# Optimization experiments

Hardware: AMD Instinct MI355X
Metric: run time of the kernel (lower is better)

The kernel has to match this reference:

```python
import jax, jax.numpy as jnp
import numpy as np

H = 1024      # hidden_size
M = 64        # matrix_dim = int(sqrt(4096))
R = 2         # rank
LS = 2048     # local_size = budget_size // 2


def setup_inputs() -> dict:
    key = jax.random.key(0)
    ks = jax.random.split(key, 12)
    B, S = 4, 2048
    def lin(k, fan_in, fan_out):
        # stored as [in, out] so forward is x @ W
        return jax.random.normal(k, (fan_in, fan_out), dtype=jnp.float32) / np.sqrt(fan_in)
    return {
        "x": jax.random.normal(ks[0], (B, S, H), dtype=jnp.float32),
        "W_decay": lin(ks[1], H, 1),
        "W_key": lin(ks[2], H, R * M),
        "W_value": lin(ks[3], H, R * M),
        "W_ql": lin(ks[4], H, M),
        "W_qr": lin(ks[5], H, M),
        "W_rec_out": lin(ks[6], M, H),
        "W_up": lin(ks[7], H, LS),
        "W_gate": lin(ks[8], H, LS),
        "W_down": lin(ks[9], LS, H),
        "init_state": jnp.zeros((M, M), dtype=jnp.float32),
    }


def reference(x, W_decay, W_key, W_value, W_ql, W_qr, W_rec_out, W_up, W_gate, W_down, init_state):
    B, S, _ = x.shape
    # Precompute all per-token projections (vectorized over batch & seq)
    decay = jax.nn.sigmoid(x @ W_decay)[..., 0]            # [B,S]
    keys = (x @ W_key).reshape(B, S, R, M)                 # [B,S,R,M]
    values = (x @ W_value).reshape(B, S, R, M)             # [B,S,R,M]
    write = jnp.einsum('bsrm,bsrn->bsmn', keys, values) / float(R)  # [B,S,M,M]
    ql = x @ W_ql                                          # [B,S,M]
    qr = x @ W_qr                                          # [B,S,M]

    def step(state, inp):
        d, w, ql_t, qr_t = inp                             # d:[B], w:[B,M,M], ql/qr:[B,M]
        d3 = d[:, None, None]
        state = d3 * state + (1.0 - d3) * w                # decayed matrix-state update
        read = jnp.einsum('bm,bmn->bn', ql_t, state) * qr_t  # [B,M]
        return state, read

    state0 = jnp.broadcast_to(init_state, (B, M, M))
    # scan over time axis (time-major inputs)
    _, reads = jax.lax.scan(
        step, state0,
        (decay.transpose(1, 0), write.transpose(1, 0, 2, 3),
         ql.transpose(1, 0, 2), qr.transpose(1, 0, 2)))
    reads = reads.transpose(1, 0, 2)                       # [B,S,M]

    recurrent = jax.nn.silu(reads) @ W_rec_out             # [B,S,H]
    local = ((x @ W_up) * jax.nn.silu(x @ W_gate)) @ W_down  # SwiGLU branch
    return recurrent + local
```

## Files before the change

kernel.cpp:

```cpp
#include <hip/hip_runtime.h>
#include <hip/hip_bf16.h>

typedef __bf16 bf16x8 __attribute__((ext_vector_type(8)));
typedef float f32x4 __attribute__((ext_vector_type(4)));

#define BS   8192
#define Hd   1024
#define LSd  2048
#define Md   64

static __device__ __forceinline__ float bfu2f(unsigned short u) {
  return __uint_as_float(((unsigned int)u) << 16);
}
static __device__ __forceinline__ __hip_bfloat16 f2bf(float f) { return __float2bfloat16(f); }



__global__ __launch_bounds__(256) void conv_frag_kernel(const float* __restrict__ src,
    __hip_bfloat16* __restrict__ dst) {
  int wid = (blockIdx.x * 256 + threadIdx.x) >> 6;
  int lane = threadIdx.x & 63;
  int t = wid >> 3, ri = wid & 7;
  int mb = t >> 5, kt = t & 31;
  int row = mb * 128 + ri * 16 + (lane & 15);
  int k = kt * 32 + (lane >> 4) * 8;
  const float* s = src + (size_t)row * 1024 + k;
  float4 f0 = *(const float4*)s;
  float4 f1 = *(const float4*)(s + 4);
  union { unsigned short u8[8]; uint4 v; } o;
  o.u8[0] = __bfloat16_as_ushort(f2bf(f0.x)); o.u8[1] = __bfloat16_as_ushort(f2bf(f0.y));
  o.u8[2] = __bfloat16_as_ushort(f2bf(f0.z)); o.u8[3] = __bfloat16_as_ushort(f2bf(f0.w));
  o.u8[4] = __bfloat16_as_ushort(f2bf(f1.x)); o.u8[5] = __bfloat16_as_ushort(f2bf(f1.y));
  o.u8[6] = __bfloat16_as_ushort(f2bf(f1.z)); o.u8[7] = __bfloat16_as_ushort(f2bf(f1.w));
  *(uint4*)(dst + (size_t)wid * 512 + lane * 8) = o.v;
}

__global__ __launch_bounds__(256) void prep_wcat_frag_kernel(const float* __restrict__ Wd,
    const float* __restrict__ Wk, const float* __restrict__ Wv,
    const float* __restrict__ Wql, const float* __restrict__ Wqr,
    __hip_bfloat16* __restrict__ out) {
  int i = blockIdx.x * 256 + threadIdx.x;
  int t = i >> 12, ri = (i >> 9) & 7, l = (i >> 3) & 63, e = i & 7;
  int n = (t >> 5) * 128 + ri * 16 + (l & 15);
  int h = (t & 31) * 32 + (l >> 4) * 8 + e;
  float v = 0.f;
  if (n == 0)        v = Wd[h];
  else if (n < 129)  v = Wk[h * 128 + (n - 1)];
  else if (n < 257)  v = Wv[h * 128 + (n - 129)];
  else if (n < 321)  v = Wql[h * 64 + (n - 257)];
  else if (n < 385)  v = Wqr[h * 64 + (n - 321)];
  out[i] = f2bf(v);
}

__global__ __launch_bounds__(256) void transpose_frag_kernel(const float* __restrict__ src,
    __hip_bfloat16* __restrict__ dst, int Ktot, int Nsrc, int n_off) {
  __shared__ float tile[32][129];
  int kt = blockIdx.x, nb = blockIdx.y;
  int k0 = kt * 32, n0 = nb * 128;
  int tid = threadIdx.x;
  int kr = tid >> 3, nc = (tid & 7) * 16;
  const float* s = src + (size_t)(k0 + kr) * Nsrc + n0 + nc;
  #pragma unroll
  for (int u = 0; u < 16; u += 4) {
    float4 f = *(const float4*)(s + u);
    tile[kr][nc + u + 0] = f.x; tile[kr][nc + u + 1] = f.y;
    tile[kr][nc + u + 2] = f.z; tile[kr][nc + u + 3] = f.w;
  }
  __syncthreads();
  int wave = tid >> 6, lane = tid & 63;
  int tIdx = ((n0 + n_off) >> 7) * (Ktot >> 5) + kt;
  __hip_bfloat16* d = dst + ((size_t)tIdx << 12);
  #pragma unroll
  for (int it = 0; it < 2; ++it) {
    int ri = wave * 2 + it;
    int nl = ri * 16 + (lane & 15), kq = (lane >> 4) * 8;
    union { unsigned short u8[8]; uint4 v; } o;
    #pragma unroll
    for (int e = 0; e < 8; ++e)
      o.u8[e] = __bfloat16_as_ushort(f2bf(tile[kq + e][nl]));
    *(uint4*)(d + ri * 512 + lane * 8) = o.v;
  }
}


static __device__ __forceinline__ void stage_async_frag(const __hip_bfloat16* __restrict__ tile_src,
    __hip_bfloat16* __restrict__ dst, int wave, int lane) {
  #pragma unroll
  for (int it = 0; it < 2; ++it) {
    int ri = wave * 2 + it;
    __builtin_amdgcn_global_load_lds(
        (const __attribute__((address_space(1))) void*)(tile_src + ri * 512 + lane * 8),
        (__attribute__((address_space(3))) void*)(dst + ri * 512),
        16, 0, 0);
  }
}

static __device__ __forceinline__ void mfma_single(const __hip_bfloat16* sA, const __hip_bfloat16* sB,
    int wm16, int wn16, int lane, f32x4 acc[4][4]) {
  bf16x8 af[4], bg[4];
  #pragma unroll
  for (int i = 0; i < 4; ++i) af[i] = *(const bf16x8*)(sA + (wm16 + i) * 512 + lane * 8);
  #pragma unroll
  for (int j = 0; j < 4; ++j) bg[j] = *(const bf16x8*)(sB + (wn16 + j) * 512 + lane * 8);
  #pragma unroll
  for (int i = 0; i < 4; ++i)
    #pragma unroll
    for (int j = 0; j < 4; ++j)
      acc[i][j] = __builtin_amdgcn_mfma_f32_16x16x32_bf16(af[i], bg[j], acc[i][j], 0, 0, 0);
}

static __device__ __forceinline__ void mfma_dual(const __hip_bfloat16* sA,
    const __hip_bfloat16* sBu, const __hip_bfloat16* sBg,
    int wm16, int wn16, int lane, f32x4 accu[4][4], f32x4 accg[4][4]) {
  bf16x8 af[4], bu[4], bg[4];
  #pragma unroll
  for (int i = 0; i < 4; ++i) af[i] = *(const bf16x8*)(sA + (wm16 + i) * 512 + lane * 8);
  #pragma unroll
  for (int j = 0; j < 4; ++j) bu[j] = *(const bf16x8*)(sBu + (wn16 + j) * 512 + lane * 8);
  #pragma unroll
  for (int j = 0; j < 4; ++j) bg[j] = *(const bf16x8*)(sBg + (wn16 + j) * 512 + lane * 8);
  #pragma unroll
  for (int i = 0; i < 4; ++i)
    #pragma unroll
    for (int j = 0; j < 4; ++j) {
      accu[i][j] = __builtin_amdgcn_mfma_f32_16x16x32_bf16(af[i], bu[j], accu[i][j], 0, 0, 0);
      accg[i][j] = __builtin_amdgcn_mfma_f32_16x16x32_bf16(af[i], bg[j], accg[i][j], 0, 0, 0);
    }
}

__global__ __launch_bounds__(256, 2) void gemm_proj_kernel(const __hip_bfloat16* __restrict__ A,
    const __hip_bfloat16* __restrict__ Bt, float* __restrict__ C) {
  __shared__ __align__(16) __hip_bfloat16 sA[4096];
  __shared__ __align__(16) __hip_bfloat16 sB[4096];
  int tid = threadIdx.x, nb = blockIdx.x, mb = blockIdx.y;
  int wave = tid >> 6, lane = tid & 63;
  int wm16 = (wave >> 1) * 4, wn16 = (wave & 1) * 4;
  int fr = lane & 15, q4 = (lane >> 4) * 4;
  f32x4 acc[4][4] = {};
  for (int kt = 0; kt < 32; ++kt) {
    __syncthreads();
    stage_async_frag(A + ((size_t)(mb * 32 + kt) << 12), sA, wave, lane);
    stage_async_frag(Bt + ((size_t)(nb * 32 + kt) << 12), sB, wave, lane);
    __syncthreads();
    mfma_single(sA, sB, wm16, wn16, lane, acc);
  }
  #pragma unroll
  for (int i = 0; i < 4; ++i)
    #pragma unroll
    for (int j = 0; j < 4; ++j) {
      int row = mb * 128 + (wm16 + i) * 16 + q4;
      int col = nb * 128 + (wn16 + j) * 16 + fr;
      #pragma unroll
      for (int rg = 0; rg < 4; ++rg)
        C[(size_t)(row + rg) * 512 + col] = acc[i][j][rg];
    }
}

__global__ __launch_bounds__(256, 2) void gemm_upgate_kernel(const __hip_bfloat16* __restrict__ A,
    const __hip_bfloat16* __restrict__ Bt, __hip_bfloat16* __restrict__ hout) {
  __shared__ __align__(16) __hip_bfloat16 sA[4096];
  __shared__ __align__(16) __hip_bfloat16 sBu[4096];
  __shared__ __align__(16) __hip_bfloat16 sBg[4096];
  int tid = threadIdx.x, nb = blockIdx.x, mb = blockIdx.y;
  int wave = tid >> 6, lane = tid & 63;
  int wm16 = (wave >> 1) * 4, wn16 = (wave & 1) * 4;
  int fr = lane & 15, q4 = (lane >> 4) * 4;
  f32x4 accu[4][4] = {}, accg[4][4] = {};
  for (int kt = 0; kt < 32; ++kt) {
    __syncthreads();
    stage_async_frag(A + ((size_t)(mb * 32 + kt) << 12), sA, wave, lane);
    stage_async_frag(Bt + ((size_t)(nb * 32 + kt) << 12), sBu, wave, lane);
    stage_async_frag(Bt + ((size_t)((nb + 16) * 32 + kt) << 12), sBg, wave, lane);
    __syncthreads();
    mfma_dual(sA, sBu, sBg, wm16, wn16, lane, accu, accg);
  }
  #pragma unroll
  for (int i = 0; i < 4; ++i)
    #pragma unroll
    for (int j = 0; j < 4; ++j) {
      int col = nb * 128 + (wn16 + j) * 16 + fr;
      int q = (col >> 3) & 3, e = col & 7;
      size_t base = ((size_t)(mb * 64 + (col >> 5)) << 12) + (wm16 + i) * 512 + q * 128 + e;
      #pragma unroll
      for (int rg = 0; rg < 4; ++rg) {
        float u = accu[i][j][rg], g = accg[i][j][rg];
        float hv = u * g / (1.f + __expf(-g));
        hout[base + (q4 + rg) * 8] = f2bf(hv);
      }
    }
}

__global__ __launch_bounds__(256, 2) void gemm_final_kernel(const __hip_bfloat16* __restrict__ A,
    const __hip_bfloat16* __restrict__ Bt, const __hip_bfloat16* __restrict__ A2,
    const __hip_bfloat16* __restrict__ B2t, float* __restrict__ C) {
  __shared__ __align__(16) __hip_bfloat16 sA[4096];
  __shared__ __align__(16) __hip_bfloat16 sB[4096];
  int tid = threadIdx.x, nb = blockIdx.x, mb = blockIdx.y;
  int wave = tid >> 6, lane = tid & 63;
  int wm16 = (wave >> 1) * 4, wn16 = (wave & 1) * 4;
  int fr = lane & 15, q4 = (lane >> 4) * 4;
  f32x4 acc[4][4] = {};
  for (int kt = 0; kt < 64; ++kt) {
    __syncthreads();
    stage_async_frag(A + ((size_t)(mb * 64 + kt) << 12), sA, wave, lane);
    stage_async_frag(Bt + ((size_t)(nb * 64 + kt) << 12), sB, wave, lane);
    __syncthreads();
    mfma_single(sA, sB, wm16, wn16, lane, acc);
  }
  #pragma unroll
  for (int kt = 0; kt < 2; ++kt) {
    __syncthreads();
    stage_async_frag(A2 + ((size_t)(mb * 2 + kt) << 12), sA, wave, lane);
    stage_async_frag(B2t + ((size_t)(nb * 2 + kt) << 12), sB, wave, lane);
    __syncthreads();
    mfma_single(sA, sB, wm16, wn16, lane, acc);
  }
  #pragma unroll
  for (int i = 0; i < 4; ++i)
    #pragma unroll
    for (int j = 0; j < 4; ++j) {
      int row = mb * 128 + (wm16 + i) * 16 + q4;
      int col = nb * 128 + (wn16 + j) * 16 + fr;
      #pragma unroll
      for (int rg = 0; rg < 4; ++rg)
        C[(size_t)(row + rg) * Hd + col] = acc[i][j][rg];
    }
}


__global__ __launch_bounds__(256) void scan_chunk_kernel(const float* __restrict__ proj,
    float* __restrict__ Lam, float* __restrict__ udv, float* __restrict__ alpha,
    float* __restrict__ dS) {
  int bc = blockIdx.x, t0 = bc * 64, tid = threadIdx.x;
  __shared__ float d_s[64], ld_s[64], Lam_s[64], u_s[64];
  __shared__ __align__(16) __hip_bfloat16 k_s[128 * 64];
  __shared__ __align__(16) __hip_bfloat16 v_s[128 * 64];
  if (tid < 64) {
    float z = proj[(size_t)(t0 + tid) * 512];
    float dd = 1.f / (1.f + __expf(-z));
    float l = (z >= 0.f) ? -log1pf(__expf(-z)) : (z - log1pf(__expf(z)));
    d_s[tid] = dd; ld_s[tid] = l;
  }
  __syncthreads();
  if (tid == 0) {
    float s = 0.f;
    for (int j = 0; j < 64; ++j) { s += ld_s[j]; Lam_s[j] = s; }
  }
  __syncthreads();
  float Lend = Lam_s[63];
  if (tid < 64) {
    u_s[tid] = (1.f - d_s[tid]) * __expf(Lend - Lam_s[tid]) * 0.5f;
    Lam[t0 + tid] = Lam_s[tid];
    udv[t0 + tid] = (1.f - d_s[tid]) * 0.5f;
  }
  if (tid == 0) alpha[bc] = __expf(Lend);
  __syncthreads();
  for (int i = tid; i < 128 * 64; i += 256) {
    int jr = i >> 6, m = i & 63, j = jr >> 1, r = jr & 1;
    const float* rowp = proj + (size_t)(t0 + j) * 512;
    k_s[i] = f2bf(u_s[j] * rowp[1 + r * 64 + m]);
    v_s[i] = f2bf(rowp[129 + r * 64 + m]);
  }
  __syncthreads();
  int m0 = (tid & 15) * 4, n0 = (tid >> 4) * 4;
  float acc[4][4] = {{0.f}};
  for (int jr = 0; jr < 128; ++jr) {
    ushort4 ku = *(const ushort4*)&k_s[jr * 64 + m0];
    ushort4 vu = *(const ushort4*)&v_s[jr * 64 + n0];
    float k0 = bfu2f(ku.x), k1 = bfu2f(ku.y), k2 = bfu2f(ku.z), k3 = bfu2f(ku.w);
    float v0 = bfu2f(vu.x), v1 = bfu2f(vu.y), v2 = bfu2f(vu.z), v3 = bfu2f(vu.w);
    acc[0][0] += k0 * v0; acc[0][1] += k0 * v1; acc[0][2] += k0 * v2; acc[0][3] += k0 * v3;
    acc[1][0] += k1 * v0; acc[1][1] += k1 * v1; acc[1][2] += k1 * v2; acc[1][3] += k1 * v3;
    acc[2][0] += k2 * v0; acc[2][1] += k2 * v1; acc[2][2] += k2 * v2; acc[2][3] += k2 * v3;
    acc[3][0] += k3 * v0; acc[3][1] += k3 * v1; acc[3][2] += k3 * v2; acc[3][3] += k3 * v3;
  }
  float* outp = dS + (size_t)bc * 4096;
  #pragma unroll
  for (int a = 0; a < 4; ++a)
    #pragma unroll
    for (int b2 = 0; b2 < 4; ++b2)
      outp[(m0 + a) * 64 + (n0 + b2)] = acc[a][b2];
}

__global__ __launch_bounds__(256) void scan_cross_kernel(const float* __restrict__ dS,
    const float* __restrict__ alpha, const float* __restrict__ init_state,
    float* __restrict__ Sin) {
  int idx = blockIdx.x * 256 + threadIdx.x;
  int b = idx >> 12, e = idx & 4095;
  float s = init_state[e];
  for (int c = 0; c < 32; ++c) {
    int bc = b * 32 + c;
    Sin[(size_t)bc * 4096 + e] = s;
    s = alpha[bc] * s + dS[(size_t)bc * 4096 + e];
  }
}

#define QLD 68

__global__ __launch_bounds__(256) void scan_read_kernel(const float* __restrict__ proj,
    const float* __restrict__ Lam, const float* __restrict__ udv,
    const float* __restrict__ Sin, __hip_bfloat16* __restrict__ Rd) {
  int bc = blockIdx.x, t0 = bc * 64, tid = threadIdx.x;
  __shared__ __align__(16) __hip_bfloat16 ql_s[64 * QLD];
  __shared__ __align__(16) __hip_bfloat16 kv_s[128 * 64];
  __shared__ __align__(16) __hip_bfloat16 S_s[64 * 64];
  __shared__ __align__(16) __hip_bfloat16 P_s[128 * 64];
  __shared__ float Lam_s[64], ud_s[64], eL_s[64];
  for (int i = tid; i < 64 * 64; i += 256) {
    int t = i >> 6, m = i & 63;
    ql_s[t * QLD + m] = f2bf(proj[(size_t)(t0 + t) * 512 + 257 + m]);
    S_s[i] = f2bf(Sin[(size_t)bc * 4096 + i]);
  }
  for (int i = tid; i < 128 * 64; i += 256) {
    int jr = i >> 6, m = i & 63, j = jr >> 1, r = jr & 1;
    kv_s[i] = f2bf(proj[(size_t)(t0 + j) * 512 + 1 + r * 64 + m]);
  }
  if (tid < 64) {
    float L = Lam[t0 + tid];
    Lam_s[tid] = L; ud_s[tid] = udv[t0 + tid]; eL_s[tid] = __expf(L);
  }
  __syncthreads();
  int tr = (tid & 15) * 4, n0 = (tid >> 4) * 4;
  float acc[4][4] = {{0.f}};
  for (int mb4 = 0; mb4 < 64; mb4 += 4) {
    float sm[4][4];
    #pragma unroll
    for (int mm = 0; mm < 4; ++mm) {
      ushort4 sv = *(const ushort4*)&S_s[(mb4 + mm) * 64 + n0];
      sm[mm][0] = bfu2f(sv.x); sm[mm][1] = bfu2f(sv.y);
      sm[mm][2] = bfu2f(sv.z); sm[mm][3] = bfu2f(sv.w);
    }
    #pragma unroll
    for (int a = 0; a < 4; ++a) {
      ushort4 qa = *(const ushort4*)&ql_s[(tr + a) * QLD + mb4];
      float q0 = bfu2f(qa.x), q1 = bfu2f(qa.y), q2 = bfu2f(qa.z), q3 = bfu2f(qa.w);
      #pragma unroll
      for (int b2 = 0; b2 < 4; ++b2)
        acc[a][b2] += q0 * sm[0][b2] + q1 * sm[1][b2] + q2 * sm[2][b2] + q3 * sm[3][b2];
    }
  }
  #pragma unroll
  for (int a = 0; a < 4; ++a) {
    float e = eL_s[tr + a];
    #pragma unroll
    for (int b2 = 0; b2 < 4; ++b2) acc[a][b2] *= e;
  }
  {
    int jr = tid >> 1, j = jr >> 1, tb = (tid & 1) * 32;
    float dot[32];
    #pragma unroll
    for (int t2 = 0; t2 < 32; ++t2) dot[t2] = 0.f;
    for (int m = 0; m < 64; m += 4) {
      ushort4 kb = *(const ushort4*)&kv_s[jr * 64 + m];
      float k0 = bfu2f(kb.x), k1 = bfu2f(kb.y), k2 = bfu2f(kb.z), k3 = bfu2f(kb.w);
      #pragma unroll
      for (int t2 = 0; t2 < 32; ++t2) {
        ushort4 qa = *(const ushort4*)&ql_s[(tb + t2) * QLD + m];
        dot[t2] += bfu2f(qa.x) * k0 + bfu2f(qa.y) * k1 + bfu2f(qa.z) * k2 + bfu2f(qa.w) * k3;
      }
    }
    #pragma unroll
    for (int t2 = 0; t2 < 32; ++t2) {
      int t = tb + t2;
      float coef = (j <= t) ? ud_s[j] * __expf(Lam_s[t] - Lam_s[j]) : 0.f;
      P_s[jr * 64 + t] = f2bf(dot[t2] * coef);
    }
  }
  __syncthreads();
  for (int i = tid; i < 128 * 64; i += 256) {
    int jr = i >> 6, m = i & 63, j = jr >> 1, r = jr & 1;
    kv_s[i] = f2bf(proj[(size_t)(t0 + j) * 512 + 129 + r * 64 + m]);
  }
  __syncthreads();
  for (int jr = 0; jr < 128; ++jr) {
    ushort4 pu = *(const ushort4*)&P_s[jr * 64 + tr];
    ushort4 vu = *(const ushort4*)&kv_s[jr * 64 + n0];
    float p0 = bfu2f(pu.x), p1 = bfu2f(pu.y), p2 = bfu2f(pu.z), p3 = bfu2f(pu.w);
    float v0 = bfu2f(vu.x), v1 = bfu2f(vu.y), v2 = bfu2f(vu.z), v3 = bfu2f(vu.w);
    acc[0][0] += p0 * v0; acc[0][1] += p0 * v1; acc[0][2] += p0 * v2; acc[0][3] += p0 * v3;
    acc[1][0] += p1 * v0; acc[1][1] += p1 * v1; acc[1][2] += p1 * v2; acc[1][3] += p1 * v3;
    acc[2][0] += p2 * v0; acc[2][1] += p2 * v1; acc[2][2] += p2 * v2; acc[2][3] += p2 * v3;
    acc[3][0] += p3 * v0; acc[3][1] += p3 * v1; acc[3][2] += p3 * v2; acc[3][3] += p3 * v3;
  }
  #pragma unroll
  for (int a = 0; a < 4; ++a) {
    int row = t0 + tr + a;
    const float* qrp = proj + (size_t)row * 512 + 321;
    int tBase = (row >> 7) * 2, ri = (row >> 4) & 7, rl = row & 15;
    #pragma unroll
    for (int b2 = 0; b2 < 4; ++b2) {
      int n = n0 + b2;
      float rv = acc[a][b2] * qrp[n];
      float sv = rv / (1.f + __expf(-rv));
      size_t idx = ((size_t)(tBase + (n >> 5)) << 12) + ri * 512
                 + (rl + ((n >> 3) & 3) * 16) * 8 + (n & 7);
      Rd[idx] = f2bf(sv);
    }
  }
}


extern "C" void kernel_launch(void* const* d_in, const int* in_sizes, int n_in,
                              void* d_out, int out_size, void* d_ws, size_t ws_size,
                              hipStream_t stream) {
  const float* x      = (const float*)d_in[0];
  const float* W_dec  = (const float*)d_in[1];
  const float* W_key  = (const float*)d_in[2];
  const float* W_val  = (const float*)d_in[3];
  const float* W_ql   = (const float*)d_in[4];
  const float* W_qr   = (const float*)d_in[5];
  const float* W_rec  = (const float*)d_in[6];
  const float* W_up   = (const float*)d_in[7];
  const float* W_gate = (const float*)d_in[8];
  const float* W_down = (const float*)d_in[9];
  const float* init_state = (const float*)d_in[10];
  float* out = (float*)d_out;

  char* w = (char*)d_ws;
  auto take = [&](size_t bytes) { char* p = w; w += (bytes + 255) & ~(size_t)255; return p; };
  __hip_bfloat16* x_fb   = (__hip_bfloat16*)take((size_t)BS * Hd * 2);
  __hip_bfloat16* Wcat_f = (__hip_bfloat16*)take((size_t)512 * Hd * 2);
  __hip_bfloat16* Wug_f  = (__hip_bfloat16*)take((size_t)4096 * Hd * 2);
  __hip_bfloat16* Wdn_f  = (__hip_bfloat16*)take((size_t)Hd * LSd * 2);
  __hip_bfloat16* Wrc_f  = (__hip_bfloat16*)take((size_t)Hd * Md * 2);
  float* proj  = (float*)take((size_t)BS * 512 * 4);
  float* Lam   = (float*)take((size_t)BS * 4);
  float* udv   = (float*)take((size_t)BS * 4);
  float* alpha = (float*)take((size_t)128 * 4);
  float* dS    = (float*)take((size_t)128 * 4096 * 4);
  float* Sin   = (float*)take((size_t)128 * 4096 * 4);
  __hip_bfloat16* Rd   = (__hip_bfloat16*)take((size_t)BS * Md * 2);
  __hip_bfloat16* hbuf = (__hip_bfloat16*)take((size_t)BS * LSd * 2);

  conv_frag_kernel<<<4096, 256, 0, stream>>>(x, x_fb);
  prep_wcat_frag_kernel<<<2048, 256, 0, stream>>>(W_dec, W_key, W_val, W_ql, W_qr, Wcat_f);
  transpose_frag_kernel<<<dim3(32, 16), 256, 0, stream>>>(W_up,   Wug_f, Hd, LSd, 0);
  transpose_frag_kernel<<<dim3(32, 16), 256, 0, stream>>>(W_gate, Wug_f, Hd, LSd, 2048);
  transpose_frag_kernel<<<dim3(64, 8),  256, 0, stream>>>(W_down, Wdn_f, LSd, Hd, 0);
  transpose_frag_kernel<<<dim3(2, 8),   256, 0, stream>>>(W_rec,  Wrc_f, Md, Hd, 0);

  gemm_proj_kernel<<<dim3(4, 64), 256, 0, stream>>>(x_fb, Wcat_f, proj);

  scan_chunk_kernel<<<128, 256, 0, stream>>>(proj, Lam, udv, alpha, dS);
  scan_cross_kernel<<<64, 256, 0, stream>>>(dS, alpha, init_state, Sin);
  scan_read_kernel<<<128, 256, 0, stream>>>(proj, Lam, udv, Sin, Rd);

  gemm_upgate_kernel<<<dim3(16, 64), 256, 0, stream>>>(x_fb, Wug_f, hbuf);
  gemm_final_kernel<<<dim3(8, 64), 256, 0, stream>>>(hbuf, Wdn_f, Rd, Wrc_f, out);
}
```

Measured before the change: 318.8 us.

## Double K-step per barrier in GEMMs, swap grid order, merge weight transposes

Each GEMM kernel now stages two K tiles (64-wide) per pair of barriers instead of one, halving the number of __syncthreads and doubling LDS usage per block. Grid dimensions are swapped so consecutive blocks share the same weight column block (M varies fastest), changing L2 reuse patterns. The four weight-transpose launches are merged into one kernel with block-index dispatch to cut launch overhead. Larger LDS footprint (up to 48KB for upgate) may reduce occupancy.

```diff
diff --git a/kernel.cpp b/kernel.cpp
--- a/kernel.cpp
+++ b/kernel.cpp
@@ -52,10 +52,18 @@
   out[i] = f2bf(v);
 }
 
-__global__ __launch_bounds__(256) void transpose_frag_kernel(const float* __restrict__ src,
-    __hip_bfloat16* __restrict__ dst, int Ktot, int Nsrc, int n_off) {
+__global__ __launch_bounds__(256) void transpose_all_kernel(
+    const float* __restrict__ Wup, const float* __restrict__ Wgate,
+    const float* __restrict__ Wdown, const float* __restrict__ Wrec,
+    __hip_bfloat16* __restrict__ Wug_f, __hip_bfloat16* __restrict__ Wdn_f,
+    __hip_bfloat16* __restrict__ Wrc_f) {
   __shared__ float tile[32][129];
-  int kt = blockIdx.x, nb = blockIdx.y;
+  int b = blockIdx.x;
+  const float* src; __hip_bfloat16* dst; int Ktot, Nsrc, n_off, kt, nb;
+  if (b < 512)        { src = Wup;   dst = Wug_f; Ktot = 1024; Nsrc = 2048; n_off = 0;    int r = b;        kt = r & 31; nb = r >> 5; }
+  else if (b < 1024)  { src = Wgate; dst = Wug_f; Ktot = 1024; Nsrc = 2048; n_off = 2048; int r = b - 512;  kt = r & 31; nb = r >> 5; }
+  else if (b < 1536)  { src = Wdown; dst = Wdn_f; Ktot = 2048; Nsrc = 1024; n_off = 0;    int r = b - 1024; kt = r & 63; nb = r >> 6; }
+  else                { src = Wrec;  dst = Wrc_f; Ktot = 64;   Nsrc = 1024; n_off = 0;    int r = b - 1536; kt = r & 1;  nb = r >> 1; }
   int k0 = kt * 32, n0 = nb * 128;
   int tid = threadIdx.x;
   int kr = tid >> 3, nc = (tid & 7) * 16;
@@ -130,19 +138,22 @@
 
 __global__ __launch_bounds__(256, 2) void gemm_proj_kernel(const __hip_bfloat16* __restrict__ A,
     const __hip_bfloat16* __restrict__ Bt, float* __restrict__ C) {
-  __shared__ __align__(16) __hip_bfloat16 sA[4096];
-  __shared__ __align__(16) __hip_bfloat16 sB[4096];
-  int tid = threadIdx.x, nb = blockIdx.x, mb = blockIdx.y;
+  __shared__ __align__(16) __hip_bfloat16 sA[8192];
+  __shared__ __align__(16) __hip_bfloat16 sB[8192];
+  int tid = threadIdx.x, mb = blockIdx.x, nb = blockIdx.y;
   int wave = tid >> 6, lane = tid & 63;
   int wm16 = (wave >> 1) * 4, wn16 = (wave & 1) * 4;
   int fr = lane & 15, q4 = (lane >> 4) * 4;
   f32x4 acc[4][4] = {};
-  for (int kt = 0; kt < 32; ++kt) {
+  for (int kt = 0; kt < 32; kt += 2) {
     __syncthreads();
     stage_async_frag(A + ((size_t)(mb * 32 + kt) << 12), sA, wave, lane);
+    stage_async_frag(A + ((size_t)(mb * 32 + kt + 1) << 12), sA + 4096, wave, lane);
     stage_async_frag(Bt + ((size_t)(nb * 32 + kt) << 12), sB, wave, lane);
+    stage_async_frag(Bt + ((size_t)(nb * 32 + kt + 1) << 12), sB + 4096, wave, lane);
     __syncthreads();
     mfma_single(sA, sB, wm16, wn16, lane, acc);
+    mfma_single(sA + 4096, sB + 4096, wm16, wn16, lane, acc);
   }
   #pragma unroll
   for (int i = 0; i < 4; ++i)
@@ -158,21 +169,25 @@
 
 __global__ __launch_bounds__(256, 2) void gemm_upgate_kernel(const __hip_bfloat16* __restrict__ A,
     const __hip_bfloat16* __restrict__ Bt, __hip_bfloat16* __restrict__ hout) {
-  __shared__ __align__(16) __hip_bfloat16 sA[4096];
-  __shared__ __align__(16) __hip_bfloat16 sBu[4096];
-  __shared__ __align__(16) __hip_bfloat16 sBg[4096];
-  int tid = threadIdx.x, nb = blockIdx.x, mb = blockIdx.y;
+  __shared__ __align__(16) __hip_bfloat16 sA[8192];
+  __shared__ __align__(16) __hip_bfloat16 sBu[8192];
+  __shared__ __align__(16) __hip_bfloat16 sBg[8192];
+  int tid = threadIdx.x, mb = blockIdx.x, nb = blockIdx.y;
   int wave = tid >> 6, lane = tid & 63;
   int wm16 = (wave >> 1) * 4, wn16 = (wave & 1) * 4;
   int fr = lane & 15, q4 = (lane >> 4) * 4;
   f32x4 accu[4][4] = {}, accg[4][4] = {};
-  for (int kt = 0; kt < 32; ++kt) {
+  for (int kt = 0; kt < 32; kt += 2) {
     __syncthreads();
     stage_async_frag(A + ((size_t)(mb * 32 + kt) << 12), sA, wave, lane);
+    stage_async_frag(A + ((size_t)(mb * 32 + kt + 1) << 12), sA + 4096, wave, lane);
     stage_async_frag(Bt + ((size_t)(nb * 32 + kt) << 12), sBu, wave, lane);
+    stage_async_frag(Bt + ((size_t)(nb * 32 + kt + 1) << 12), sBu + 4096, wave, lane);
     stage_async_frag(Bt + ((size_t)((nb + 16) * 32 + kt) << 12), sBg, wave, lane);
+    stage_async_frag(Bt + ((size_t)((nb + 16) * 32 + kt + 1) << 12), sBg + 4096, wave, lane);
     __syncthreads();
     mfma_dual(sA, sBu, sBg, wm16, wn16, lane, accu, accg);
+    mfma_dual(sA + 4096, sBu + 4096, sBg + 4096, wm16, wn16, lane, accu, accg);
   }
   #pragma unroll
   for (int i = 0; i < 4; ++i)
@@ -193,27 +208,32 @@
 __global__ __launch_bounds__(256, 2) void gemm_final_kernel(const __hip_bfloat16* __restrict__ A,
     const __hip_bfloat16* __restrict__ Bt, const __hip_bfloat16* __restrict__ A2,
     const __hip_bfloat16* __restrict__ B2t, float* __restrict__ C) {
-  __shared__ __align__(16) __hip_bfloat16 sA[4096];
-  __shared__ __align__(16) __hip_bfloat16 sB[4096];
-  int tid = threadIdx.x, nb = blockIdx.x, mb = blockIdx.y;
+  __shared__ __align__(16) __hip_bfloat16 sA[8192];
+  __shared__ __align__(16) __hip_bfloat16 sB[8192];
+  int tid = threadIdx.x, mb = blockIdx.x, nb = blockIdx.y;
   int wave = tid >> 6, lane = tid & 63;
   int wm16 = (wave >> 1) * 4, wn16 = (wave & 1) * 4;
   int fr = lane & 15, q4 = (lane >> 4) * 4;
   f32x4 acc[4][4] = {};
-  for (int kt = 0; kt < 64; ++kt) {
+  for (int kt = 0; kt < 64; kt += 2) {
     __syncthreads();
     stage_async_frag(A + ((size_t)(mb * 64 + kt) << 12), sA, wave, lane);
+    stage_async_frag(A + ((size_t)(mb * 64 + kt + 1) << 12), sA + 4096, wave, lane);
     stage_async_frag(Bt + ((size_t)(nb * 64 + kt) << 12), sB, wave, lane);
+    stage_async_frag(Bt + ((size_t)(nb * 64 + kt + 1) << 12), sB + 4096, wave, lane);
     __syncthreads();
     mfma_single(sA, sB, wm16, wn16, lane, acc);
-  }
-  #pragma unroll
-  for (int kt = 0; kt < 2; ++kt) {
-    __syncthreads();
-    stage_async_frag(A2 + ((size_t)(mb * 2 + kt) << 12), sA, wave, lane);
-    stage_async_frag(B2t + ((size_t)(nb * 2 + kt) << 12), sB, wave, lane);
+    mfma_single(sA + 4096, sB + 4096, wm16, wn16, lane, acc);
+  }
+  {
+    __syncthreads();
+    stage_async_frag(A2 + ((size_t)(mb * 2) << 12), sA, wave, lane);
+    stage_async_frag(A2 + ((size_t)(mb * 2 + 1) << 12), sA + 4096, wave, lane);
+    stage_async_frag(B2t + ((size_t)(nb * 2) << 12), sB, wave, lane);
+    stage_async_frag(B2t + ((size_t)(nb * 2 + 1) << 12), sB + 4096, wave, lane);
     __syncthreads();
     mfma_single(sA, sB, wm16, wn16, lane, acc);
+    mfma_single(sA + 4096, sB + 4096, wm16, wn16, lane, acc);
   }
   #pragma unroll
   for (int i = 0; i < 4; ++i)
@@ -434,17 +454,15 @@
 
   conv_frag_kernel<<<4096, 256, 0, stream>>>(x, x_fb);
   prep_wcat_frag_kernel<<<2048, 256, 0, stream>>>(W_dec, W_key, W_val, W_ql, W_qr, Wcat_f);
-  transpose_frag_kernel<<<dim3(32, 16), 256, 0, stream>>>(W_up,   Wug_f, Hd, LSd, 0);
-  transpose_frag_kernel<<<dim3(32, 16), 256, 0, stream>>>(W_gate, Wug_f, Hd, LSd, 2048);
-  transpose_frag_kernel<<<dim3(64, 8),  256, 0, stream>>>(W_down, Wdn_f, LSd, Hd, 0);
-  transpose_frag_kernel<<<dim3(2, 8),   256, 0, stream>>>(W_rec,  Wrc_f, Md, Hd, 0);
-
-  gemm_proj_kernel<<<dim3(4, 64), 256, 0, stream>>>(x_fb, Wcat_f, proj);
+  transpose_all_kernel<<<1552, 256, 0, stream>>>(W_up, W_gate, W_down, W_rec,
+                                                 Wug_f, Wdn_f, Wrc_f);
+
+  gemm_proj_kernel<<<dim3(64, 4), 256, 0, stream>>>(x_fb, Wcat_f, proj);
 
   scan_chunk_kernel<<<128, 256, 0, stream>>>(proj, Lam, udv, alpha, dS);
   scan_cross_kernel<<<64, 256, 0, stream>>>(dS, alpha, init_state, Sin);
   scan_read_kernel<<<128, 256, 0, stream>>>(proj, Lam, udv, Sin, Rd);
 
-  gemm_upgate_kernel<<<dim3(16, 64), 256, 0, stream>>>(x_fb, Wug_f, hbuf);
-  gemm_final_kernel<<<dim3(8, 64), 256, 0, stream>>>(hbuf, Wdn_f, Rd, Wrc_f, out);
-}
+  gemm_upgate_kernel<<<dim3(64, 16), 256, 0, stream>>>(x_fb, Wug_f, hbuf);
+  gemm_final_kernel<<<dim3(64, 8), 256, 0, stream>>>(hbuf, Wdn_f, Rd, Wrc_f, out);
+}
```

New measurement: 301.7 us. 1.06x faster.
